# Kernel tuning notes

Hardware: AMD Instinct MI355X
Metric: run time of the kernel (lower is better)

## Reference

```python
import jax, jax.numpy as jnp
import numpy as np

BATCH, OUT, M, IN = 128, 256, 8, 512

def setup_inputs() -> dict:
    key = jax.random.key(0)
    k1, k2 = jax.random.split(key)
    x = jax.random.normal(k1, (BATCH, M, IN), dtype=jnp.float32)
    DNM_W = jax.random.normal(k2, (OUT, M, IN), dtype=jnp.float32)
    return {"x": x, "DNM_W": DNM_W}

def reference(x, DNM_W):
    # broadcast mul: (i,1,j,k) * (1,b,j,k) -> (i,b,j,k)
    z = jax.nn.sigmoid(x[:, None, :, :] * DNM_W[None, :, :, :])
    z = jnp.sum(z, axis=3)   # (i,b,j): sum over input_size
    z = jnp.prod(z, axis=2)  # (i,b):   prod over M branches
    # normalize(rate=1, dim=1): scale rows to sum 1, then standardize (unbiased std)
    total = jnp.sum(z, axis=1, keepdims=True)
    z = z / total
    mean = jnp.mean(z, axis=1, keepdims=True)
    std = jnp.std(z, axis=1, keepdims=True, ddof=1)  # torch.std is unbiased
    return (z - mean) / std
```

## Files before the change

kernel.cpp:

```cpp
#include <hip/hip_runtime.h>
#include <hip/hip_bf16.h>

#define BATCH 128
#define NOUT  256
#define MB    8
#define IN    512

#define TI 16
#define TB 16
#define THREADS 256
#define CH 256
#define CH4 (CH/4)
#define STRIDE4 65

__device__ __forceinline__ float fast_exp2(float x) {
#if __has_builtin(__builtin_amdgcn_exp2f)
  return __builtin_amdgcn_exp2f(x);
#else
  return exp2f(x);
#endif
}
__device__ __forceinline__ float fast_rcp(float x) {
#if __has_builtin(__builtin_amdgcn_rcpf)
  return __builtin_amdgcn_rcpf(x);
#else
  return 1.0f / x;
#endif
}

__global__ __launch_bounds__(THREADS) void dnm_partial_kernel(
    const float* __restrict__ x, const float* __restrict__ w,
    float* __restrict__ part, int j_per_block)
{
  __shared__ float4 xs4[TI * STRIDE4];
  __shared__ float4 ws4[TB * STRIDE4];

  const int t  = threadIdx.x;
  const int ti = t >> 4;
  const int tb = t & 15;
  const int b0 = blockIdx.x * TB;
  const int i0 = blockIdx.y * TI;
  const int j0 = blockIdx.z * j_per_block;

  const float4* gx = (const float4*)x;
  const float4* gw = (const float4*)w;
  const float NEG_LOG2E = -1.4426950408889634f;

  float prod = 1.0f;
  for (int j = j0; j < j0 + j_per_block; ++j) {
    float acc0 = 0.0f, acc1 = 0.0f;
    for (int kc = 0; kc < IN / CH; ++kc) {
      __syncthreads();
      #pragma unroll
      for (int p = 0; p < (TI * CH4) / THREADS; ++p) {
        int idx = t + p * THREADS;
        int r = idx >> 6, c4 = idx & 63;
        float4 xv = gx[(size_t)((i0 + r) * MB + j) * (IN / 4) + kc * CH4 + c4];
        xv.x *= NEG_LOG2E; xv.y *= NEG_LOG2E; xv.z *= NEG_LOG2E; xv.w *= NEG_LOG2E;
        xs4[r * STRIDE4 + c4] = xv;
        ws4[r * STRIDE4 + c4] = gw[(size_t)((b0 + r) * MB + j) * (IN / 4) + kc * CH4 + c4];
      }
      __syncthreads();
      const float4* __restrict__ xr = &xs4[ti * STRIDE4];
      const float4* __restrict__ wr = &ws4[tb * STRIDE4];
      #pragma unroll 8
      for (int k4 = 0; k4 < CH4; ++k4) {
        float4 xv = xr[k4];
        float4 wv = wr[k4];
        float ea = fast_exp2(xv.x * wv.x);
        float eb = fast_exp2(xv.y * wv.y);
        float ec = fast_exp2(xv.z * wv.z);
        float ed = fast_exp2(xv.w * wv.w);
        float A = 1.0f + ea, B = 1.0f + eb, C = 1.0f + ec, D = 1.0f + ed;
        float AB = A * B, CD = C * D;
        float num = fmaf(A + B, CD, (C + D) * AB);
        float den = AB * CD;
        if (k4 & 1) acc1 = fmaf(num, fast_rcp(den), acc1);
        else        acc0 = fmaf(num, fast_rcp(den), acc0);
      }
    }
    prod *= (acc0 + acc1);
  }
  part[(size_t)blockIdx.z * (BATCH * NOUT) + (size_t)(i0 + ti) * NOUT + (b0 + tb)] = prod;
}

__device__ __forceinline__ float block_sum(float v, float* red) {
  #pragma unroll
  for (int o = 32; o > 0; o >>= 1) v += __shfl_down(v, o, 64);
  int lane = threadIdx.x & 63, wid = threadIdx.x >> 6;
  __syncthreads();
  if (lane == 0) red[wid] = v;
  __syncthreads();
  return red[0] + red[1] + red[2] + red[3];
}

__global__ __launch_bounds__(256) void dnm_norm_kernel(
    const float* __restrict__ part, float* __restrict__ out, int jg)
{
  __shared__ float red[4];
  const int i = blockIdx.x;
  const int t = threadIdx.x;
  float z = 1.0f;
  for (int g = 0; g < jg; ++g)
    z *= part[(size_t)g * (BATCH * NOUT) + (size_t)i * NOUT + t];

  float S  = block_sum(z, red);
  float zn = z / S;
  float m  = block_sum(zn, red) * (1.0f / NOUT);
  float dv = zn - m;
  float v  = block_sum(dv * dv, red) * (1.0f / (NOUT - 1));
  out[(size_t)i * NOUT + t] = dv / sqrtf(v);
}

extern "C" void kernel_launch(void* const* d_in, const int* in_sizes, int n_in,
                              void* d_out, int out_size, void* d_ws, size_t ws_size,
                              hipStream_t stream) {
  const float* x = (const float*)d_in[0];
  const float* w = (const float*)d_in[1];
  float* out = (float*)d_out;

  const size_t plane = (size_t)BATCH * NOUT * sizeof(float);
  int jg;
  float* part;
  if (ws_size >= 8 * plane)      { jg = 8; part = (float*)d_ws; }
  else if (ws_size >= 4 * plane) { jg = 4; part = (float*)d_ws; }
  else if (ws_size >= 2 * plane) { jg = 2; part = (float*)d_ws; }
  else if (ws_size >= plane)     { jg = 1; part = (float*)d_ws; }
  else                           { jg = 1; part = out; }

  const int jpb = MB / jg;
  dim3 gridA(NOUT / TB, BATCH / TI, jg);
  dnm_partial_kernel<<<gridA, THREADS, 0, stream>>>(x, w, part, jpb);
  dnm_norm_kernel<<<dim3(BATCH), 256, 0, stream>>>(part, out, jg);
}
```

Before: 88.57 us.

## Register-block 2x2 outputs per thread and split reduction over K chunks

Each thread now computes a 2x2 block of (i,b) outputs from 32x32 tiles, so every shared-memory float4 load feeds two sigmoid evaluations instead of one. The K dimension is also split across grid z (kg groups), writing partial sums that the norm kernel adds before taking the product over branches. This aims to cut LDS traffic per transcendental and keep parallelism up with larger tiles, at the cost of more workspace, extra partial-sum reads and more register pressure.

```diff
diff --git a/kernel.cpp b/kernel.cpp
--- a/kernel.cpp
+++ b/kernel.cpp
@@ -6,82 +6,102 @@
 #define MB    8
 #define IN    512
 
-#define TI 16
-#define TB 16
 #define THREADS 256
-#define CH 256
+#define TI 32
+#define TB 32
+#define CH 128
 #define CH4 (CH/4)
-#define STRIDE4 65
+#define ST4 33
 
-__device__ __forceinline__ float fast_exp2(float x) {
+__device__ __forceinline__ float fast_exp2(float v) {
 #if __has_builtin(__builtin_amdgcn_exp2f)
-  return __builtin_amdgcn_exp2f(x);
+  return __builtin_amdgcn_exp2f(v);
 #else
-  return exp2f(x);
+  return exp2f(v);
 #endif
 }
-__device__ __forceinline__ float fast_rcp(float x) {
+__device__ __forceinline__ float fast_rcp(float v) {
 #if __has_builtin(__builtin_amdgcn_rcpf)
-  return __builtin_amdgcn_rcpf(x);
+  return __builtin_amdgcn_rcpf(v);
 #else
-  return 1.0f / x;
+  return 1.0f / v;
 #endif
 }
 
-__global__ __launch_bounds__(THREADS) void dnm_partial_kernel(
+__device__ __forceinline__ float sig4(float4 p) {
+  float ea = fast_exp2(p.x), eb = fast_exp2(p.y), ec = fast_exp2(p.z), ed = fast_exp2(p.w);
+  float A = 1.0f + ea, B = 1.0f + eb, C = 1.0f + ec, D = 1.0f + ed;
+  float AB = A * B, CD = C * D;
+  float num = fmaf(A + B, CD, (C + D) * AB);
+  return num * fast_rcp(AB * CD);
+}
+__device__ __forceinline__ float4 mul4(float4 a, float4 b) {
+  return make_float4(a.x * b.x, a.y * b.y, a.z * b.z, a.w * b.w);
+}
+
+__global__ __launch_bounds__(THREADS, 4) void dnm_partial_kernel(
     const float* __restrict__ x, const float* __restrict__ w,
-    float* __restrict__ part, int j_per_block)
+    float* __restrict__ part, int jpb, int kcb)
 {
-  __shared__ float4 xs4[TI * STRIDE4];
-  __shared__ float4 ws4[TB * STRIDE4];
+  __shared__ float4 xs4[TI * ST4];
+  __shared__ float4 ws4[TB * ST4];
 
-  const int t  = threadIdx.x;
-  const int ti = t >> 4;
-  const int tb = t & 15;
-  const int b0 = blockIdx.x * TB;
-  const int i0 = blockIdx.y * TI;
-  const int j0 = blockIdx.z * j_per_block;
+  const int t   = threadIdx.x;
+  const int ti2 = t >> 4;
+  const int tb2 = t & 15;
+  const int b0  = blockIdx.x * TB;
+  const int i0  = blockIdx.y * TI;
+  const int kg  = (IN / CH) / kcb;
+  const int j0  = (blockIdx.z / kg) * jpb;
+  const int q0  = (blockIdx.z % kg) * kcb;
 
   const float4* gx = (const float4*)x;
   const float4* gw = (const float4*)w;
   const float NEG_LOG2E = -1.4426950408889634f;
 
-  float prod = 1.0f;
-  for (int j = j0; j < j0 + j_per_block; ++j) {
-    float acc0 = 0.0f, acc1 = 0.0f;
-    for (int kc = 0; kc < IN / CH; ++kc) {
+  float p00 = 1.0f, p01 = 1.0f, p10 = 1.0f, p11 = 1.0f;
+  for (int jj = 0; jj < jpb; ++jj) {
+    const int j = j0 + jj;
+    float s00 = 0.0f, s01 = 0.0f, s10 = 0.0f, s11 = 0.0f;
+    for (int cc = 0; cc < kcb; ++cc) {
+      const int q = q0 + cc;
       __syncthreads();
       #pragma unroll
-      for (int p = 0; p < (TI * CH4) / THREADS; ++p) {
+      for (int p = 0; p < (2 * TI * CH4) / THREADS; ++p) {
         int idx = t + p * THREADS;
-        int r = idx >> 6, c4 = idx & 63;
-        float4 xv = gx[(size_t)((i0 + r) * MB + j) * (IN / 4) + kc * CH4 + c4];
-        xv.x *= NEG_LOG2E; xv.y *= NEG_LOG2E; xv.z *= NEG_LOG2E; xv.w *= NEG_LOG2E;
-        xs4[r * STRIDE4 + c4] = xv;
-        ws4[r * STRIDE4 + c4] = gw[(size_t)((b0 + r) * MB + j) * (IN / 4) + kc * CH4 + c4];
+        int r = idx >> 5, c4 = idx & 31;
+        if (r < TI) {
+          float4 xv = gx[(size_t)((i0 + r) * MB + j) * (IN / 4) + q * CH4 + c4];
+          xv.x *= NEG_LOG2E; xv.y *= NEG_LOG2E; xv.z *= NEG_LOG2E; xv.w *= NEG_LOG2E;
+          xs4[r * ST4 + c4] = xv;
+        } else {
+          ws4[(r - TI) * ST4 + c4] =
+              gw[(size_t)((b0 + r - TI) * MB + j) * (IN / 4) + q * CH4 + c4];
+        }
       }
       __syncthreads();
-      const float4* __restrict__ xr = &xs4[ti * STRIDE4];
-      const float4* __restrict__ wr = &ws4[tb * STRIDE4];
-      #pragma unroll 8
+      const float4* __restrict__ xr0 = &xs4[(2 * ti2)     * ST4];
+      const float4* __restrict__ xr1 = &xs4[(2 * ti2 + 1) * ST4];
+      const float4* __restrict__ wr0 = &ws4[(2 * tb2)     * ST4];
+      const float4* __restrict__ wr1 = &ws4[(2 * tb2 + 1) * ST4];
+      #pragma unroll 2
       for (int k4 = 0; k4 < CH4; ++k4) {
-        float4 xv = xr[k4];
-        float4 wv = wr[k4];
-        float ea = fast_exp2(xv.x * wv.x);
-        float eb = fast_exp2(xv.y * wv.y);
-        float ec = fast_exp2(xv.z * wv.z);
-        float ed = fast_exp2(xv.w * wv.w);
-        float A = 1.0f + ea, B = 1.0f + eb, C = 1.0f + ec, D = 1.0f + ed;
-        float AB = A * B, CD = C * D;
-        float num = fmaf(A + B, CD, (C + D) * AB);
-        float den = AB * CD;
-        if (k4 & 1) acc1 = fmaf(num, fast_rcp(den), acc1);
-        else        acc0 = fmaf(num, fast_rcp(den), acc0);
+        float4 xv0 = xr0[k4], xv1 = xr1[k4];
+        float4 wv0 = wr0[k4], wv1 = wr1[k4];
+        s00 += sig4(mul4(xv0, wv0));
+        s01 += sig4(mul4(xv0, wv1));
+        s10 += sig4(mul4(xv1, wv0));
+        s11 += sig4(mul4(xv1, wv1));
       }
     }
-    prod *= (acc0 + acc1);
+    p00 *= s00; p01 *= s01; p10 *= s10; p11 *= s11;
   }
-  part[(size_t)blockIdx.z * (BATCH * NOUT) + (size_t)(i0 + ti) * NOUT + (b0 + tb)] = prod;
+  float* dst = part + (size_t)blockIdx.z * (BATCH * NOUT);
+  const int i = i0 + 2 * ti2, b = b0 + 2 * tb2;
+  dst[(size_t)i * NOUT + b]           = p00;
+  dst[(size_t)i * NOUT + b + 1]       = p01;
+  dst[(size_t)(i + 1) * NOUT + b]     = p10;
+  dst[(size_t)(i + 1) * NOUT + b + 1] = p11;
 }
 
 __device__ __forceinline__ float block_sum(float v, float* red) {
@@ -95,15 +115,18 @@
 }
 
 __global__ __launch_bounds__(256) void dnm_norm_kernel(
-    const float* __restrict__ part, float* __restrict__ out, int jg)
+    const float* __restrict__ part, float* __restrict__ out, int jg, int kg)
 {
   __shared__ float red[4];
   const int i = blockIdx.x;
   const int t = threadIdx.x;
   float z = 1.0f;
-  for (int g = 0; g < jg; ++g)
-    z *= part[(size_t)g * (BATCH * NOUT) + (size_t)i * NOUT + t];
-
+  for (int j = 0; j < jg; ++j) {
+    float s = 0.0f;
+    for (int q = 0; q < kg; ++q)
+      s += part[(size_t)(j * kg + q) * (BATCH * NOUT) + (size_t)i * NOUT + t];
+    z *= s;
+  }
   float S  = block_sum(z, red);
   float zn = z / S;
   float m  = block_sum(zn, red) * (1.0f / NOUT);
@@ -120,16 +143,17 @@
   float* out = (float*)d_out;
 
   const size_t plane = (size_t)BATCH * NOUT * sizeof(float);
-  int jg;
+  int jg, kg;
   float* part;
-  if (ws_size >= 8 * plane)      { jg = 8; part = (float*)d_ws; }
-  else if (ws_size >= 4 * plane) { jg = 4; part = (float*)d_ws; }
-  else if (ws_size >= 2 * plane) { jg = 2; part = (float*)d_ws; }
-  else if (ws_size >= plane)     { jg = 1; part = (float*)d_ws; }
-  else                           { jg = 1; part = out; }
+  if      (ws_size >= 32 * plane) { jg = 8; kg = 4; part = (float*)d_ws; }
+  else if (ws_size >= 16 * plane) { jg = 8; kg = 2; part = (float*)d_ws; }
+  else if (ws_size >=  8 * plane) { jg = 8; kg = 1; part = (float*)d_ws; }
+  else if (ws_size >=      plane) { jg = 1; kg = 1; part = (float*)d_ws; }
+  else                            { jg = 1; kg = 1; part = out; }
 
   const int jpb = MB / jg;
-  dim3 gridA(NOUT / TB, BATCH / TI, jg);
-  dnm_partial_kernel<<<gridA, THREADS, 0, stream>>>(x, w, part, jpb);
-  dnm_norm_kernel<<<dim3(BATCH), 256, 0, stream>>>(part, out, jg);
+  const int kcb = (IN / CH) / kg;
+  dim3 gridA(NOUT / TB, BATCH / TI, jg * kg);
+  dnm_partial_kernel<<<gridA, THREADS, 0, stream>>>(x, w, part, jpb, kcb);
+  dnm_norm_kernel<<<dim3(BATCH), 256, 0, stream>>>(part, out, jg, kg);
 }
```

New measurement: 90.19 us. No clear change (+1.8%).
